# Performance work log

Hardware: AMD Instinct MI355X
Metric: run time of the kernel (lower is better)

The kernel has to match this reference:

```python
import jax, jax.numpy as jnp
import numpy as np

B, W, E, P, H, NH = 2, 512, 2, 8, 1024, 16
D = H // NH  # 64
T = W + E


def _split_heads(x):
    # [..., S, H] -> [..., NH, S, D]
    x = x.reshape(x.shape[:-1] + (NH, D))
    return jnp.swapaxes(x, -2, -3)


def setup_inputs() -> dict:
    key = jax.random.key(0)
    ks = jax.random.split(key, 16)
    s = 0.02
    inp = {
        "word_hidden_states": jax.random.normal(ks[0], (B, W, H), jnp.float32),
        "entity_hidden_states": jax.random.normal(ks[1], (B, P, E, H), jnp.float32),
        "attention_mask": jnp.zeros((B, 1, 1, T), jnp.float32),
        "q_w": jax.random.normal(ks[2], (H, H), jnp.float32) * s,
        "q_b": jnp.zeros((H,), jnp.float32),
        "k_w": jax.random.normal(ks[3], (H, H), jnp.float32) * s,
        "k_b": jnp.zeros((H,), jnp.float32),
        "v_w": jax.random.normal(ks[4], (H, H), jnp.float32) * s,
        "v_b": jnp.zeros((H,), jnp.float32),
        "w2e_w": jax.random.normal(ks[5], (H, H), jnp.float32) * s,
        "w2e_b": jnp.zeros((H,), jnp.float32),
        "e2w_w": jax.random.normal(ks[6], (H, H), jnp.float32) * s,
        "e2w_b": jnp.zeros((H,), jnp.float32),
        "e2e_w": jax.random.normal(ks[7], (H, H), jnp.float32) * s,
        "e2e_b": jnp.zeros((H,), jnp.float32),
    }
    return inp


def reference(word_hidden_states, entity_hidden_states, attention_mask,
              q_w, q_b, k_w, k_b, v_w, v_b,
              w2e_w, w2e_b, e2w_w, e2w_b, e2e_w, e2e_b):
    words = word_hidden_states          # [B, W, H]
    ents = entity_hidden_states         # [B, P, E, H]

    # Queries: words use `query` and `w2e_query`; entities use `e2w_query` and `e2e_query`.
    w2w_q = _split_heads(words @ q_w + q_b)      # [B, NH, W, D]
    w2e_q = _split_heads(words @ w2e_w + w2e_b)  # [B, NH, W, D]
    e2w_q = _split_heads(ents @ e2w_w + e2w_b)   # [B, P, NH, E, D]
    e2e_q = _split_heads(ents @ e2e_w + e2e_b)   # [B, P, NH, E, D]

    # Shared key/value projection on [expanded words ; entities]. Word K/V are
    # identical across pairs (expand), so compute once and broadcast.
    k_word = _split_heads(words @ k_w + k_b)     # [B, NH, W, D]
    k_ent = _split_heads(ents @ k_w + k_b)       # [B, P, NH, E, D]
    v_word = _split_heads(words @ v_w + v_b)     # [B, NH, W, D]
    v_ent = _split_heads(ents @ v_w + v_b)       # [B, P, NH, E, D]

    # Four block score matrices.
    s_w2w = jnp.einsum('bhqd,bhkd->bhqk', w2w_q, k_word)      # [B, NH, W, W]
    s_w2e = jnp.einsum('bhqd,bphkd->bphqk', w2e_q, k_ent)     # [B, P, NH, W, E]
    s_e2w = jnp.einsum('bphqd,bhkd->bphqk', e2w_q, k_word)    # [B, P, NH, E, W]
    s_e2e = jnp.einsum('bphqd,bphkd->bphqk', e2e_q, k_ent)    # [B, P, NH, E, E]

    word_scores = jnp.concatenate(
        [jnp.broadcast_to(s_w2w[:, None], (B, P, NH, W, W)), s_w2e], axis=-1)
    ent_scores = jnp.concatenate([s_e2w, s_e2e], axis=-1)
    scores = jnp.concatenate([word_scores, ent_scores], axis=-2)  # [B, P, NH, T, T]

    scale = jnp.asarray(1.0 / np.sqrt(D), scores.dtype)
    scores = scores * scale + attention_mask[:, None]  # mask broadcasts [B,1,1,1,T]
    probs = jax.nn.softmax(scores, axis=-1)  # dropout: eval mode (deterministic)

    v = jnp.concatenate(
        [jnp.broadcast_to(v_word[:, None], (B, P, NH, W, D)), v_ent], axis=-2)
    ctx = jnp.einsum('bphqk,bphkd->bphqd', probs, v)   # [B, P, NH, T, D]
    ctx = jnp.swapaxes(ctx, -2, -3).reshape(B, P, T, H)

    word_reps = ctx[:, :, :W, :]   # [B, P, W, H]
    ent_reps = ctx[:, :, W:, :]    # [B, P, E, H]
    return (word_reps, ent_reps)
```

## Files before the change

kernel.cpp:

```cpp
#include <hip/hip_runtime.h>
#include <hip/hip_bf16.h>

typedef __attribute__((ext_vector_type(8))) short s16x8;
typedef __attribute__((ext_vector_type(4))) float fx4;
typedef __attribute__((ext_vector_type(4))) unsigned int u32x4;
typedef unsigned short u16;
typedef unsigned int   u32;
typedef unsigned long long u64;

#define DI __device__ __forceinline__


DI float bf2f(u16 x){ u32 u = ((u32)x)<<16; float f; __builtin_memcpy(&f,&u,4); return f; }
DI u16 f2bf(float f){ u32 u; __builtin_memcpy(&u,&f,4); u = (u + 0x7fffu + ((u>>16)&1u))>>16; return (u16)u; }

DI fx4 mfma_16x16x32_bf16(s16x8 a, s16x8 b, fx4 c){
  return __builtin_amdgcn_mfma_f32_16x16x32_bf16(a,b,c,0,0,0);
}

__global__ __launch_bounds__(256) void k_prep(
    const float* __restrict__ s0, const float* __restrict__ s1, const float* __restrict__ s2,
    const float* __restrict__ s3, const float* __restrict__ s4, const float* __restrict__ s5,
    u16* __restrict__ dstbase,
    const float* __restrict__ words, u16* __restrict__ Xbf,
    const float* __restrict__ ents,  u16* __restrict__ Ebf)
{
  __shared__ __align__(16) u16 tile[64][72];
  int bx = blockIdx.x, tid = threadIdx.x;
  if(bx < 1536){
    int z = bx>>8, t = bx&255;
    const float* src = (z==0)?s0:(z==1)?s1:(z==2)?s2:(z==3)?s3:(z==4)?s4:s5;
    u16* dst = dstbase + (u64)z*1048576u;
    int kt = (t&15)*64, nt = (t>>4)*64;
    #pragma unroll
    for(int it=0; it<2; ++it){
      int c = it*256 + tid;
      int r = c>>3, col = (c&7)*8;
      const float* sp = src + (u64)(kt+r)*1024u + nt + col;
      fx4 a = *(const fx4*)sp;
      fx4 b = *(const fx4*)(sp+4);
      u16 o[8];
      o[0]=f2bf(a[0]); o[1]=f2bf(a[1]); o[2]=f2bf(a[2]); o[3]=f2bf(a[3]);
      o[4]=f2bf(b[0]); o[5]=f2bf(b[1]); o[6]=f2bf(b[2]); o[7]=f2bf(b[3]);
      __builtin_memcpy(&tile[r][col], o, 16);
    }
    __syncthreads();
    #pragma unroll
    for(int it=0; it<2; ++it){
      int c = it*256 + tid;
      int nr = c>>3, kc = (c&7)*8;
      u16 tmp[8];
      #pragma unroll
      for(int j=0;j<8;++j) tmp[j] = tile[kc+j][nr];
      u32x4 v; __builtin_memcpy(&v, tmp, 16);
      *(u32x4*)(dst + (u64)(nt+nr)*1024u + kt + kc) = v;
    }
  } else {
    const float* src; u16* dst; int i;
    if(bx < 2048){ src = words; dst = Xbf; i = ((bx-1536)*256 + tid)*8; }
    else         { src = ents;  dst = Ebf; i = ((bx-2048)*256 + tid)*8; }
    fx4 a = *(const fx4*)(src+i);
    fx4 b = *(const fx4*)(src+i+4);
    u16 o[8];
    o[0]=f2bf(a[0]); o[1]=f2bf(a[1]); o[2]=f2bf(a[2]); o[3]=f2bf(a[3]);
    o[4]=f2bf(b[0]); o[5]=f2bf(b[1]); o[6]=f2bf(b[2]); o[7]=f2bf(b[3]);
    u32x4 v; __builtin_memcpy(&v,o,16);
    *(u32x4*)(dst+i)=v;
  }
}

__global__ __launch_bounds__(256) void k_proj(
    const u16* __restrict__ Xbf, const u16* __restrict__ Ebf,
    const u16* __restrict__ wtq, const u16* __restrict__ wtw2e,
    const u16* __restrict__ wtk, const u16* __restrict__ wtv,
    const u16* __restrict__ wte2w, const u16* __restrict__ wte2e,
    const float* __restrict__ qb, const float* __restrict__ w2eb,
    const float* __restrict__ kb, const float* __restrict__ vb,
    const float* __restrict__ e2wb, const float* __restrict__ e2eb,
    u16* __restrict__ Qw, u16* __restrict__ Q2e, u16* __restrict__ Kwp, u16* __restrict__ VwTp,
    u16* __restrict__ Qe2w, u16* __restrict__ Qe2e, u16* __restrict__ Kep, u16* __restrict__ VeTp)
{
  __shared__ __align__(16) u16 XL[128*64];
  __shared__ __align__(16) u16 WL[128*64];
  int tid = threadIdx.x;
  int z = blockIdx.z;
  int wv = tid>>6, lane = tid&63, l15 = lane&15, g = lane>>4;

  if(blockIdx.y < 8){
    const u16* WT  = (z==0)?wtq:(z==1)?wtw2e:(z==2)?wtk:wtv;
    const float* bias = (z==0)?qb :(z==1)?w2eb :(z==2)?kb :vb;
    u16* out       = (z==0)?Qw :(z==1)?Q2e :(z==2)?Kwp :VwTp;
    int nt = blockIdx.x*64;
    int mt = blockIdx.y*128;
    int wr = (wv>>1)*64, wc = (wv&1)*32;
    fx4 acc[4][2] = {};
    u32x4 rx[4], rw[2];
    #pragma unroll
    for(int it=0; it<4; ++it){
      int c = it*256 + tid;
      int r = c>>3, cb = (c&7)*16, scb = cb ^ ((r&7)<<4);
      rx[it] = *(const u32x4*)((const char*)Xbf + ((u64)(mt+r)*1024u)*2u + scb);
    }
    #pragma unroll
    for(int it=0; it<2; ++it){
      int c = it*256 + tid;
      int r = c>>3, cb = (c&7)*16, scb = cb ^ ((r&7)<<4);
      rw[it] = *(const u32x4*)((const char*)WT + ((u64)(nt+r)*1024u)*2u + scb);
    }
    #pragma unroll
    for(int it=0; it<4; ++it) *(u32x4*)((char*)XL + (it*256+tid)*16) = rx[it];
    #pragma unroll
    for(int it=0; it<2; ++it) *(u32x4*)((char*)WL + (it*256+tid)*16) = rw[it];
    __syncthreads();
    for(int t=0; t<16; ++t){
      int kn = (t+1)*64;
      if(t < 15){
        #pragma unroll
        for(int it=0; it<4; ++it){
          int c = it*256 + tid;
          int r = c>>3, cb = (c&7)*16, scb = cb ^ ((r&7)<<4);
          rx[it] = *(const u32x4*)((const char*)Xbf + ((u64)(mt+r)*1024u + kn)*2u + scb);
        }
        #pragma unroll
        for(int it=0; it<2; ++it){
          int c = it*256 + tid;
          int r = c>>3, cb = (c&7)*16, scb = cb ^ ((r&7)<<4);
          rw[it] = *(const u32x4*)((const char*)WT + ((u64)(nt+r)*1024u + kn)*2u + scb);
        }
      }
      #pragma unroll
      for(int ks=0; ks<2; ++ks){
        s16x8 af[4], bfv[2];
        #pragma unroll
        for(int i=0;i<4;++i){
          int ra = wr + i*16 + l15;
          af[i]  = *(const s16x8*)((const char*)XL + ra*128 + ((ks*64 + g*16) ^ ((ra&7)<<4)));
        }
        #pragma unroll
        for(int j=0;j<2;++j){
          int rb = wc + j*16 + l15;
          bfv[j] = *(const s16x8*)((const char*)WL + rb*128 + ((ks*64 + g*16) ^ ((rb&7)<<4)));
        }
        #pragma unroll
        for(int i=0;i<4;++i)
          #pragma unroll
          for(int j=0;j<2;++j)
            acc[i][j] = mfma_16x16x32_bf16(af[i], bfv[j], acc[i][j]);
      }
      __syncthreads();
      if(t < 15){
        #pragma unroll
        for(int it=0; it<4; ++it) *(u32x4*)((char*)XL + (it*256+tid)*16) = rx[it];
        #pragma unroll
        for(int it=0; it<2; ++it) *(u32x4*)((char*)WL + (it*256+tid)*16) = rw[it];
        __syncthreads();
      }
    }
    bool vmode = (z==3);
    #pragma unroll
    for(int j=0;j<2;++j){
      int n = nt + wc + j*16 + l15;
      float bv = bias[n];
      int h = n>>6, d = n&63;
      #pragma unroll
      for(int i=0;i<4;++i){
        #pragma unroll
        for(int q=0;q<4;++q){
          int m = mt + wr + i*16 + g*4 + q;
          int bb = m>>9, wrow = m&511;
          float v = acc[i][j][q] + bv;
          u64 o = vmode ? (((u64)(bb*16+h)*64u + d)*512u + wrow)
                        : (((u64)(bb*16+h)*512u + wrow)*64u + d);
          out[o] = f2bf(v);
        }
      }
    }
  } else {
    if(blockIdx.x >= 8) return;
    const u16* WT  = (z==0)?wte2w:(z==1)?wte2e:(z==2)?wtk:wtv;
    const float* bias = (z==0)?e2wb :(z==1)?e2eb :(z==2)?kb :vb;
    u16* out       = (z==0)?Qe2w :(z==1)?Qe2e :(z==2)?Kep :VeTp;
    int nt = blockIdx.x*128;
    int wc = wv*32;
    fx4 acc[2][2] = {};
    for(int kk=0; kk<1024; kk+=64){
      {
        int r = tid>>3, cb = (tid&7)*16, scb = cb ^ ((r&7)<<4);
        *(u32x4*)((char*)XL + r*128 + cb) =
          *(const u32x4*)((const char*)Ebf + ((u64)r*1024u + kk)*2u + scb);
      }
      #pragma unroll
      for(int it=0; it<4; ++it){
        int c = it*256 + tid;
        int r = c>>3, cb = (c&7)*16, scb = cb ^ ((r&7)<<4);
        *(u32x4*)((char*)WL + r*128 + cb) =
          *(const u32x4*)((const char*)WT + ((u64)(nt+r)*1024u + kk)*2u + scb);
      }
      __syncthreads();
      #pragma unroll
      for(int ks=0; ks<2; ++ks){
        s16x8 af[2], bfv[2];
        #pragma unroll
        for(int i=0;i<2;++i){
          int ra = i*16 + l15;
          af[i]  = *(const s16x8*)((const char*)XL + ra*128 + ((ks*64 + g*16) ^ ((ra&7)<<4)));
          int rb = wc + i*16 + l15;
          bfv[i] = *(const s16x8*)((const char*)WL + rb*128 + ((ks*64 + g*16) ^ ((rb&7)<<4)));
        }
        #pragma unroll
        for(int i=0;i<2;++i)
          #pragma unroll
          for(int j=0;j<2;++j)
            acc[i][j] = mfma_16x16x32_bf16(af[i], bfv[j], acc[i][j]);
      }
      __syncthreads();
    }
    bool vmode = (z==3);
    #pragma unroll
    for(int j=0;j<2;++j){
      int n = nt + wc + j*16 + l15;
      float bv = bias[n];
      int h = n>>6, d = n&63;
      #pragma unroll
      for(int i=0;i<2;++i){
        #pragma unroll
        for(int q=0;q<4;++q){
          int m = i*16 + g*4 + q;
          int bb = m>>4, p = (m>>1)&7, e = m&1;
          float v = acc[i][j][q] + bv;
          u64 base = ((u64)(bb*8+p)*16u + h);
          u64 o = vmode ? ((base*64u + d)*2u + e)
                        : ((base*2u + e)*64u + d);
          out[o] = f2bf(v);
        }
      }
    }
  }
}

__global__ __launch_bounds__(256) void k_attn(
    const u16* __restrict__ Qw,  const u16* __restrict__ Q2e,
    const u16* __restrict__ Kw,  const u16* __restrict__ VwT,
    const u16* __restrict__ Ke,  const u16* __restrict__ VeT,
    const u16* __restrict__ Qe2w, const u16* __restrict__ Qe2e,
    const float* __restrict__ msk, float* __restrict__ outw, float* __restrict__ oute)
{
  const float scale = 0.125f;
  __shared__ __align__(16) u16 KL[64*64];
  __shared__ __align__(16) u16 VtL[64*64];
  __shared__ __align__(16) u16 PT[4][64][18];
  __shared__ __align__(16) float mask_lds[576];
  __shared__ __align__(16) float obuf[4][16][68];
  __shared__ float s_lds[2][516];
  __shared__ float red[2][8];
  int tid = threadIdx.x;
  int h = blockIdx.y, b = blockIdx.z;
  int wv = tid>>6, lane = tid&63, l15 = lane&15, g = lane>>4;

  if(blockIdx.x < 8){
    int qc = blockIdx.x;
    int q0 = qc*64 + wv*16;

    for(int i=tid;i<576;i+=256) mask_lds[i] = (i<514) ? msk[b*514+i] : 0.f;

    const u16* Qrow = Qw + ((u64)(b*16+h)*512u + q0 + l15)*64u;
    s16x8 qf0 = *(const s16x8*)(Qrow + g*8);
    s16x8 qf1 = *(const s16x8*)(Qrow + 32 + g*8);

    const char* Kpan = (const char*)(Kw  + (u64)(b*16+h)*512u*64u);
    const char* Vpan = (const char*)(VwT + (u64)(b*16+h)*64u*512u);

    float m_run = -3.0e38f, l_run = 0.f;
    fx4 oacc[4] = {};
    int swz = (l15&7)<<4;

    u32x4 rk[2], rv[2];
    #pragma unroll
    for(int it=0; it<2; ++it){
      int cc = it*256 + tid;
      int r = cc>>3, cb = (cc&7)*16, scb = cb ^ ((r&7)<<4);
      rk[it] = *(const u32x4*)(Kpan + (u64)r*128u + scb);
      rv[it] = *(const u32x4*)(Vpan + (u64)r*1024u + scb);
    }
    #pragma unroll
    for(int it=0; it<2; ++it){
      int cc = it*256 + tid;
      int r = cc>>3, cb = (cc&7)*16;
      *(u32x4*)((char*)KL  + r*128 + cb) = rk[it];
      *(u32x4*)((char*)VtL + r*128 + cb) = rv[it];
    }
    __syncthreads();

    for(int c=0;c<8;++c){
      if(c < 7){
        #pragma unroll
        for(int it=0; it<2; ++it){
          int cc = it*256 + tid;
          int r = cc>>3, cb = (cc&7)*16, scb = cb ^ ((r&7)<<4);
          rk[it] = *(const u32x4*)(Kpan + (u64)((c+1)*64+r)*128u + scb);
          rv[it] = *(const u32x4*)(Vpan + (u64)r*1024u + (u64)(c+1)*128u + scb);
        }
      }
      float sv[4][4];
      #pragma unroll
      for(int s=0;s<4;++s){
        int rk_ = (s*16 + l15)*128;
        s16x8 ka0 = *(const s16x8*)((const char*)KL + rk_ + ((g*16) ^ swz));
        s16x8 ka1 = *(const s16x8*)((const char*)KL + rk_ + ((64 + g*16) ^ swz));
        fx4 st = {0.f,0.f,0.f,0.f};
        st = mfma_16x16x32_bf16(ka0, qf0, st);
        st = mfma_16x16x32_bf16(ka1, qf1, st);
        fx4 mk = *(const fx4*)&mask_lds[c*64 + s*16 + g*4];
        #pragma unroll
        for(int q=0;q<4;++q) sv[s][q] = st[q]*scale + mk[q];
      }
      float cm = -3.0e38f;
      #pragma unroll
      for(int s=0;s<4;++s)
        #pragma unroll
        for(int q=0;q<4;++q) cm = fmaxf(cm, sv[s][q]);
      cm = fmaxf(cm, __shfl_xor(cm, 16, 64));
      cm = fmaxf(cm, __shfl_xor(cm, 32, 64));
      float m_new = fmaxf(m_run, cm);
      float alpha = __expf(m_run - m_new);
      float rs = 0.f;
      #pragma unroll
      for(int s=0;s<4;++s){
        #pragma unroll
        for(int q=0;q<4;++q){
          float e = __expf(sv[s][q] - m_new);
          rs += e;
          PT[wv][s*16 + g*4 + q][l15] = f2bf(e);
        }
      }
      rs += __shfl_xor(rs, 16, 64);
      rs += __shfl_xor(rs, 32, 64);
      l_run = l_run*alpha + rs;
      m_run = m_new;
      #pragma unroll
      for(int t=0;t<4;++t) oacc[t] *= alpha;
      asm volatile("s_waitcnt lgkmcnt(0)" ::: "memory");
      #pragma unroll
      for(int kh=0;kh<2;++kh){
        u16 ptmp[8];
        #pragma unroll
        for(int j=0;j<8;++j) ptmp[j] = PT[wv][kh*32 + g*8 + j][l15];
        s16x8 pbig; __builtin_memcpy(&pbig, ptmp, 16);
        #pragma unroll
        for(int t=0;t<4;++t){
          int rv_ = (t*16 + l15)*128;
          s16x8 va = *(const s16x8*)((const char*)VtL + rv_ + ((kh*64 + g*16) ^ swz));
          oacc[t] = mfma_16x16x32_bf16(va, pbig, oacc[t]);
        }
      }
      __syncthreads();
      if(c < 7){
        #pragma unroll
        for(int it=0; it<2; ++it){
          int cc = it*256 + tid;
          int r = cc>>3, cb = (cc&7)*16;
          *(u32x4*)((char*)KL  + r*128 + cb) = rk[it];
          *(u32x4*)((char*)VtL + r*128 + cb) = rv[it];
        }
        __syncthreads();
      }
    }

    #pragma unroll
    for(int t=0;t<4;++t)
      #pragma unroll
      for(int q=0;q<4;++q)
        obuf[wv][l15][t*16 + g*4 + q] = oacc[t][q];
    asm volatile("s_waitcnt lgkmcnt(0)" ::: "memory");

    int r = lane>>2, cbo = (lane&3)*16;
    fx4 N0 = *(const fx4*)&obuf[wv][r][cbo];
    fx4 N1 = *(const fx4*)&obuf[wv][r][cbo+4];
    fx4 N2 = *(const fx4*)&obuf[wv][r][cbo+8];
    fx4 N3 = *(const fx4*)&obuf[wv][r][cbo+12];
    float m_r = __shfl(m_run, r, 64);
    float l_r = __shfl(l_run, r, 64);
    float mke0 = mask_lds[512], mke1 = mask_lds[513];

    const u16* q2p = Q2e + ((u64)(b*16+h)*512u + q0 + r)*64u + cbo;
    float q2v[16];
    {
      s16x8 qa = *(const s16x8*)q2p;
      s16x8 qb2 = *(const s16x8*)(q2p+8);
      #pragma unroll
      for(int j=0;j<8;++j){ q2v[j]=bf2f((u16)qa[j]); q2v[8+j]=bf2f((u16)qb2[j]); }
    }

    for(int p=0;p<8;++p){
      const u16* KeP = Ke + ((u64)(b*8+p)*16u + h)*128u;
      float d0=0.f, d1=0.f;
      {
        const u16* k0p = KeP + cbo;
        const u16* k1p = KeP + 64 + cbo;
        s16x8 a0 = *(const s16x8*)k0p, a1 = *(const s16x8*)(k0p+8);
        s16x8 b0 = *(const s16x8*)k1p, b1 = *(const s16x8*)(k1p+8);
        #pragma unroll
        for(int j=0;j<8;++j){
          d0 += q2v[j]*bf2f((u16)a0[j]) + q2v[8+j]*bf2f((u16)a1[j]);
          d1 += q2v[j]*bf2f((u16)b0[j]) + q2v[8+j]*bf2f((u16)b1[j]);
        }
      }
      d0 += __shfl_xor(d0, 1, 64); d0 += __shfl_xor(d0, 2, 64);
      d1 += __shfl_xor(d1, 1, 64); d1 += __shfl_xor(d1, 2, 64);
      float s0 = d0*scale + mke0, s1 = d1*scale + mke1;
      float mp = fmaxf(m_r, fmaxf(s0, s1));
      float al = __expf(m_r - mp);
      float p0 = __expf(s0-mp), p1 = __expf(s1-mp);
      float linv = 1.0f/(l_r*al + p0 + p1);
      const u16* vep = VeT + ((u64)(b*8+p)*16u + h)*128u + cbo*2;
      u16 ve[32];
      {
        u32x4 w0 = *(const u32x4*)vep;
        u32x4 w1 = *(const u32x4*)(vep+8);
        u32x4 w2 = *(const u32x4*)(vep+16);
        u32x4 w3 = *(const u32x4*)(vep+24);
        __builtin_memcpy(ve,    &w0, 16);
        __builtin_memcpy(ve+8,  &w1, 16);
        __builtin_memcpy(ve+16, &w2, 16);
        __builtin_memcpy(ve+24, &w3, 16);
      }
      float o[16];
      #pragma unroll
      for(int j=0;j<4;++j){
        o[j]    = (N0[j]*al + p0*bf2f(ve[2*j])      + p1*bf2f(ve[2*j+1]))*linv;
        o[4+j]  = (N1[j]*al + p0*bf2f(ve[8+2*j])    + p1*bf2f(ve[8+2*j+1]))*linv;
        o[8+j]  = (N2[j]*al + p0*bf2f(ve[16+2*j])   + p1*bf2f(ve[16+2*j+1]))*linv;
        o[12+j] = (N3[j]*al + p0*bf2f(ve[24+2*j])   + p1*bf2f(ve[24+2*j+1]))*linv;
      }
      float* og = outw + ((u64)(b*8+p)*512u + q0 + r)*1024u + h*64 + cbo;
      *(fx4*)og      = *(const fx4*)&o[0];
      *(fx4*)(og+4)  = *(const fx4*)&o[4];
      *(fx4*)(og+8)  = *(const fx4*)&o[8];
      *(fx4*)(og+12) = *(const fx4*)&o[12];
    }
  } else {
    int p = blockIdx.x - 8;
    u64 ebase = (u64)(b*8+p)*16u + h;
    float* qw_lds = (float*)KL;
    float* qe_lds = (float*)VtL;
    if(tid < 128){
      int r = tid>>6, d = tid&63;
      qw_lds[r*64+d] = bf2f(Qe2w[(ebase*2 + r)*64 + d]);
      qe_lds[r*64+d] = bf2f(Qe2e[(ebase*2 + r)*64 + d]);
    }
    __syncthreads();
    const u16* Kpan = Kw + (u64)(b*16+h)*512u*64u;
    for(int k=tid;k<512;k+=256){
      const u16* kr = Kpan + (u64)k*64u;
      float d0=0.f, d1=0.f;
      #pragma unroll
      for(int j=0;j<64;j+=8){
        s16x8 kv = *(const s16x8*)(kr+j);
        #pragma unroll
        for(int x=0;x<8;++x){
          float kf = bf2f((u16)kv[x]);
          d0 += qw_lds[j+x]*kf;
          d1 += qw_lds[64+j+x]*kf;
        }
      }
      float mk = msk[b*514 + k];
      s_lds[0][k] = d0*0.125f + mk;
      s_lds[1][k] = d1*0.125f + mk;
    }
    if(tid < 4){
      int r = tid>>1, e = tid&1;
      const u16* kr = Ke + (ebase*2 + e)*64;
      float dd = 0.f;
      for(int j=0;j<64;++j) dd += qe_lds[r*64+j]*bf2f(kr[j]);
      s_lds[r][512+e] = dd*0.125f + msk[b*514 + 512 + e];
    }
    __syncthreads();
    float mx0=-3e38f, mx1=-3e38f;
    for(int k=tid;k<514;k+=256){ mx0=fmaxf(mx0,s_lds[0][k]); mx1=fmaxf(mx1,s_lds[1][k]); }
    #pragma unroll
    for(int off=32; off; off>>=1){
      mx0 = fmaxf(mx0, __shfl_xor(mx0, off, 64));
      mx1 = fmaxf(mx1, __shfl_xor(mx1, off, 64));
    }
    if(lane==0){ red[0][wv]=mx0; red[1][wv]=mx1; }
    __syncthreads();
    float m0 = fmaxf(fmaxf(red[0][0],red[0][1]),fmaxf(red[0][2],red[0][3]));
    float m1 = fmaxf(fmaxf(red[1][0],red[1][1]),fmaxf(red[1][2],red[1][3]));
    float sm0=0.f, sm1=0.f;
    for(int k=tid;k<514;k+=256){
      float e0 = __expf(s_lds[0][k]-m0); s_lds[0][k]=e0; sm0+=e0;
      float e1 = __expf(s_lds[1][k]-m1); s_lds[1][k]=e1; sm1+=e1;
    }
    #pragma unroll
    for(int off=32; off; off>>=1){
      sm0 += __shfl_xor(sm0, off, 64);
      sm1 += __shfl_xor(sm1, off, 64);
    }
    if(lane==0){ red[0][4+wv]=sm0; red[1][4+wv]=sm1; }
    __syncthreads();
    float l0 = red[0][4]+red[0][5]+red[0][6]+red[0][7];
    float l1 = red[1][4]+red[1][5]+red[1][6]+red[1][7];
    if(tid < 128){
      int r = tid>>6, d = tid&63;
      const u16* vr = VwT + ((u64)(b*16+h)*64u + d)*512u;
      float acc = 0.f;
      for(int k=0;k<512;k+=8){
        s16x8 vv = *(const s16x8*)(vr+k);
        #pragma unroll
        for(int x=0;x<8;++x) acc += s_lds[r][k+x]*bf2f((u16)vv[x]);
      }
      const u16* ve = VeT + (ebase*64 + d)*2;
      acc += s_lds[r][512]*bf2f(ve[0]) + s_lds[r][513]*bf2f(ve[1]);
      float val = acc / ((r==0)?l0:l1);
      oute[(((u64)(b*8+p)*2u + r)*1024u + h*64 + d)] = val;
    }
  }
}

extern "C" void kernel_launch(void* const* d_in, const int* in_sizes, int n_in,
                              void* d_out, int out_size, void* d_ws, size_t ws_size,
                              hipStream_t stream)
{
  const float* words = (const float*)d_in[0];
  const float* ents  = (const float*)d_in[1];
  const float* amask = (const float*)d_in[2];
  const float* q_w   = (const float*)d_in[3];
  const float* q_b   = (const float*)d_in[4];
  const float* k_w   = (const float*)d_in[5];
  const float* k_b   = (const float*)d_in[6];
  const float* v_w   = (const float*)d_in[7];
  const float* v_b   = (const float*)d_in[8];
  const float* w2e_w = (const float*)d_in[9];
  const float* w2e_b = (const float*)d_in[10];
  const float* e2w_w = (const float*)d_in[11];
  const float* e2w_b = (const float*)d_in[12];
  const float* e2e_w = (const float*)d_in[13];
  const float* e2e_b = (const float*)d_in[14];

  const size_t MW = 1048576;
  u16* ws16 = (u16*)d_ws;
  if(ws_size < (11*MW + 5*32768)*sizeof(u16)) return;
  u16* WTq   = ws16 + 0*MW;
  u16* WTk   = ws16 + 1*MW;
  u16* WTv   = ws16 + 2*MW;
  u16* WTw2e = ws16 + 3*MW;
  u16* WTe2w = ws16 + 4*MW;
  u16* WTe2e = ws16 + 5*MW;
  u16* Qw    = ws16 + 6*MW;
  u16* Q2e   = ws16 + 7*MW;
  u16* Kwp   = ws16 + 8*MW;
  u16* VwTp  = ws16 + 9*MW;
  u16* Xbf   = ws16 + 10*MW;
  u16* Qe2w  = ws16 + 11*MW;
  u16* Qe2e  = Qe2w + 32768;
  u16* Kep   = Qe2e + 32768;
  u16* VeTp  = Kep + 32768;
  u16* Ebf   = VeTp + 32768;

  dim3 tb(256);
  k_prep<<<dim3(2064), tb, 0, stream>>>(q_w, k_w, v_w, w2e_w, e2w_w, e2e_w, ws16,
                                        words, Xbf, ents, Ebf);
  k_proj<<<dim3(16,9,4), tb, 0, stream>>>(Xbf, Ebf,
      WTq, WTw2e, WTk, WTv, WTe2w, WTe2e,
      q_b, w2e_b, k_b, v_b, e2w_b, e2e_b,
      Qw, Q2e, Kwp, VwTp, Qe2w, Qe2e, Kep, VeTp);
  k_attn<<<dim3(16,16,2), tb, 0, stream>>>(Qw, Q2e, Kwp, VwTp, Kep, VeTp,
      Qe2w, Qe2e, amask, (float*)d_out, (float*)d_out + 8388608u);
}
```

Baseline: 65.27 us.

## Double-buffer LDS tiles with direct global-to-LDS loads in projection and attention

Replaces the register-staged prefetch (global load into registers, then LDS store after a barrier) with double-buffered LDS tiles filled by global_load_lds, in both the word projection GEMM and the word attention K/V loop. The goal is to remove the VGPR staging, the extra LDS write pass and one barrier per iteration, letting the next tile's loads overlap with the current MFMAs. It doubles LDS use for these buffers, which may lower occupancy. Correctness depends on the async LDS writes being complete at the single per-iteration __syncthreads, since no explicit vmcnt wait is added.

```diff
diff --git a/kernel.cpp b/kernel.cpp
--- a/kernel.cpp
+++ b/kernel.cpp
@@ -16,6 +16,12 @@
 
 DI fx4 mfma_16x16x32_bf16(s16x8 a, s16x8 b, fx4 c){
   return __builtin_amdgcn_mfma_f32_16x16x32_bf16(a,b,c,0,0,0);
+}
+
+DI void gload16(const void* g, void* l){
+  __builtin_amdgcn_global_load_lds(
+      (const __attribute__((address_space(1))) unsigned int*)g,
+      (__attribute__((address_space(3))) unsigned int*)l, 16, 0, 0);
 }
 
 __global__ __launch_bounds__(256) void k_prep(
@@ -80,8 +86,8 @@
     u16* __restrict__ Qw, u16* __restrict__ Q2e, u16* __restrict__ Kwp, u16* __restrict__ VwTp,
     u16* __restrict__ Qe2w, u16* __restrict__ Qe2e, u16* __restrict__ Kep, u16* __restrict__ VeTp)
 {
-  __shared__ __align__(16) u16 XL[128*64];
-  __shared__ __align__(16) u16 WL[128*64];
+  __shared__ __align__(16) u16 XL2[2][128*64];
+  __shared__ __align__(16) u16 WL2[2][64*64];
   int tid = threadIdx.x;
   int z = blockIdx.z;
   int wv = tid>>6, lane = tid&63, l15 = lane&15, g = lane>>4;
@@ -94,52 +100,42 @@
     int mt = blockIdx.y*128;
     int wr = (wv>>1)*64, wc = (wv&1)*32;
     fx4 acc[4][2] = {};
-    u32x4 rx[4], rw[2];
-    #pragma unroll
-    for(int it=0; it<4; ++it){
-      int c = it*256 + tid;
-      int r = c>>3, cb = (c&7)*16, scb = cb ^ ((r&7)<<4);
-      rx[it] = *(const u32x4*)((const char*)Xbf + ((u64)(mt+r)*1024u)*2u + scb);
-    }
-    #pragma unroll
-    for(int it=0; it<2; ++it){
-      int c = it*256 + tid;
-      int r = c>>3, cb = (c&7)*16, scb = cb ^ ((r&7)<<4);
-      rw[it] = *(const u32x4*)((const char*)WT + ((u64)(nt+r)*1024u)*2u + scb);
-    }
-    #pragma unroll
-    for(int it=0; it<4; ++it) *(u32x4*)((char*)XL + (it*256+tid)*16) = rx[it];
-    #pragma unroll
-    for(int it=0; it<2; ++it) *(u32x4*)((char*)WL + (it*256+tid)*16) = rw[it];
-    __syncthreads();
+
+    auto STAGE = [&](int t, int buf){
+      int kk = t*64;
+      #pragma unroll
+      for(int it=0;it<4;++it){
+        int c = it*256+tid; int r=c>>3, cb=(c&7)*16, scb=cb^((r&7)<<4);
+        gload16((const char*)Xbf + ((u64)(mt+r)*1024u + kk)*2u + scb,
+                (char*)XL2[buf] + c*16);
+      }
+      #pragma unroll
+      for(int it=0;it<2;++it){
+        int c = it*256+tid; int r=c>>3, cb=(c&7)*16, scb=cb^((r&7)<<4);
+        gload16((const char*)WT + ((u64)(nt+r)*1024u + kk)*2u + scb,
+                (char*)WL2[buf] + c*16);
+      }
+    };
+
+    STAGE(0, 0);
+    __syncthreads();
+    int cur = 0;
     for(int t=0; t<16; ++t){
-      int kn = (t+1)*64;
-      if(t < 15){
-        #pragma unroll
-        for(int it=0; it<4; ++it){
-          int c = it*256 + tid;
-          int r = c>>3, cb = (c&7)*16, scb = cb ^ ((r&7)<<4);
-          rx[it] = *(const u32x4*)((const char*)Xbf + ((u64)(mt+r)*1024u + kn)*2u + scb);
-        }
-        #pragma unroll
-        for(int it=0; it<2; ++it){
-          int c = it*256 + tid;
-          int r = c>>3, cb = (c&7)*16, scb = cb ^ ((r&7)<<4);
-          rw[it] = *(const u32x4*)((const char*)WT + ((u64)(nt+r)*1024u + kn)*2u + scb);
-        }
-      }
+      if(t < 15) STAGE(t+1, cur^1);
+      const char* XB = (const char*)XL2[cur];
+      const char* WB = (const char*)WL2[cur];
       #pragma unroll
       for(int ks=0; ks<2; ++ks){
         s16x8 af[4], bfv[2];
         #pragma unroll
         for(int i=0;i<4;++i){
           int ra = wr + i*16 + l15;
-          af[i]  = *(const s16x8*)((const char*)XL + ra*128 + ((ks*64 + g*16) ^ ((ra&7)<<4)));
+          af[i]  = *(const s16x8*)(XB + ra*128 + ((ks*64 + g*16) ^ ((ra&7)<<4)));
         }
         #pragma unroll
         for(int j=0;j<2;++j){
           int rb = wc + j*16 + l15;
-          bfv[j] = *(const s16x8*)((const char*)WL + rb*128 + ((ks*64 + g*16) ^ ((rb&7)<<4)));
+          bfv[j] = *(const s16x8*)(WB + rb*128 + ((ks*64 + g*16) ^ ((rb&7)<<4)));
         }
         #pragma unroll
         for(int i=0;i<4;++i)
@@ -148,13 +144,7 @@
             acc[i][j] = mfma_16x16x32_bf16(af[i], bfv[j], acc[i][j]);
       }
       __syncthreads();
-      if(t < 15){
-        #pragma unroll
-        for(int it=0; it<4; ++it) *(u32x4*)((char*)XL + (it*256+tid)*16) = rx[it];
-        #pragma unroll
-        for(int it=0; it<2; ++it) *(u32x4*)((char*)WL + (it*256+tid)*16) = rw[it];
-        __syncthreads();
-      }
+      cur ^= 1;
     }
     bool vmode = (z==3);
     #pragma unroll
@@ -180,20 +170,22 @@
     const u16* WT  = (z==0)?wte2w:(z==1)?wte2e:(z==2)?wtk:wtv;
     const float* bias = (z==0)?e2wb :(z==1)?e2eb :(z==2)?kb :vb;
     u16* out       = (z==0)?Qe2w :(z==1)?Qe2e :(z==2)?Kep :VeTp;
+    char* XLe = (char*)XL2;
+    char* WLe = (char*)WL2;
     int nt = blockIdx.x*128;
     int wc = wv*32;
     fx4 acc[2][2] = {};
     for(int kk=0; kk<1024; kk+=64){
       {
         int r = tid>>3, cb = (tid&7)*16, scb = cb ^ ((r&7)<<4);
-        *(u32x4*)((char*)XL + r*128 + cb) =
+        *(u32x4*)(XLe + r*128 + cb) =
           *(const u32x4*)((const char*)Ebf + ((u64)r*1024u + kk)*2u + scb);
       }
       #pragma unroll
       for(int it=0; it<4; ++it){
         int c = it*256 + tid;
         int r = c>>3, cb = (c&7)*16, scb = cb ^ ((r&7)<<4);
-        *(u32x4*)((char*)WL + r*128 + cb) =
+        *(u32x4*)(WLe + r*128 + cb) =
           *(const u32x4*)((const char*)WT + ((u64)(nt+r)*1024u + kk)*2u + scb);
       }
       __syncthreads();
@@ -203,9 +195,9 @@
         #pragma unroll
         for(int i=0;i<2;++i){
           int ra = i*16 + l15;
-          af[i]  = *(const s16x8*)((const char*)XL + ra*128 + ((ks*64 + g*16) ^ ((ra&7)<<4)));
+          af[i]  = *(const s16x8*)(XLe + ra*128 + ((ks*64 + g*16) ^ ((ra&7)<<4)));
           int rb = wc + i*16 + l15;
-          bfv[i] = *(const s16x8*)((const char*)WL + rb*128 + ((ks*64 + g*16) ^ ((rb&7)<<4)));
+          bfv[i] = *(const s16x8*)(WLe + rb*128 + ((ks*64 + g*16) ^ ((rb&7)<<4)));
         }
         #pragma unroll
         for(int i=0;i<2;++i)
@@ -246,8 +238,8 @@
     const float* __restrict__ msk, float* __restrict__ outw, float* __restrict__ oute)
 {
   const float scale = 0.125f;
-  __shared__ __align__(16) u16 KL[64*64];
-  __shared__ __align__(16) u16 VtL[64*64];
+  __shared__ __align__(16) u16 KL2[2][64*64];
+  __shared__ __align__(16) u16 VtL2[2][64*64];
   __shared__ __align__(16) u16 PT[4][64][18];
   __shared__ __align__(16) float mask_lds[576];
   __shared__ __align__(16) float obuf[4][16][68];
@@ -261,52 +253,41 @@
     int qc = blockIdx.x;
     int q0 = qc*64 + wv*16;
 
+    const char* Kpan = (const char*)(Kw  + (u64)(b*16+h)*512u*64u);
+    const char* Vpan = (const char*)(VwT + (u64)(b*16+h)*64u*512u);
+
+    auto STAGEC = [&](int c, int buf){
+      #pragma unroll
+      for(int it=0;it<2;++it){
+        int cc = it*256+tid; int r=cc>>3, cb=(cc&7)*16, scb=cb^((r&7)<<4);
+        gload16(Kpan + (u64)(c*64+r)*128u + scb, (char*)KL2[buf] + cc*16);
+        gload16(Vpan + (u64)r*1024u + (u64)c*128u + scb, (char*)VtL2[buf] + cc*16);
+      }
+    };
+
+    STAGEC(0, 0);
     for(int i=tid;i<576;i+=256) mask_lds[i] = (i<514) ? msk[b*514+i] : 0.f;
 
     const u16* Qrow = Qw + ((u64)(b*16+h)*512u + q0 + l15)*64u;
     s16x8 qf0 = *(const s16x8*)(Qrow + g*8);
     s16x8 qf1 = *(const s16x8*)(Qrow + 32 + g*8);
 
-    const char* Kpan = (const char*)(Kw  + (u64)(b*16+h)*512u*64u);
-    const char* Vpan = (const char*)(VwT + (u64)(b*16+h)*64u*512u);
-
     float m_run = -3.0e38f, l_run = 0.f;
     fx4 oacc[4] = {};
     int swz = (l15&7)<<4;
-
-    u32x4 rk[2], rv[2];
-    #pragma unroll
-    for(int it=0; it<2; ++it){
-      int cc = it*256 + tid;
-      int r = cc>>3, cb = (cc&7)*16, scb = cb ^ ((r&7)<<4);
-      rk[it] = *(const u32x4*)(Kpan + (u64)r*128u + scb);
-      rv[it] = *(const u32x4*)(Vpan + (u64)r*1024u + scb);
-    }
-    #pragma unroll
-    for(int it=0; it<2; ++it){
-      int cc = it*256 + tid;
-      int r = cc>>3, cb = (cc&7)*16;
-      *(u32x4*)((char*)KL  + r*128 + cb) = rk[it];
-      *(u32x4*)((char*)VtL + r*128 + cb) = rv[it];
-    }
-    __syncthreads();
-
+    __syncthreads();
+
+    int cur = 0;
     for(int c=0;c<8;++c){
-      if(c < 7){
-        #pragma unroll
-        for(int it=0; it<2; ++it){
-          int cc = it*256 + tid;
-          int r = cc>>3, cb = (cc&7)*16, scb = cb ^ ((r&7)<<4);
-          rk[it] = *(const u32x4*)(Kpan + (u64)((c+1)*64+r)*128u + scb);
-          rv[it] = *(const u32x4*)(Vpan + (u64)r*1024u + (u64)(c+1)*128u + scb);
-        }
-      }
+      if(c < 7) STAGEC(c+1, cur^1);
+      const char* KB = (const char*)KL2[cur];
+      const char* VB = (const char*)VtL2[cur];
       float sv[4][4];
       #pragma unroll
       for(int s=0;s<4;++s){
         int rk_ = (s*16 + l15)*128;
-        s16x8 ka0 = *(const s16x8*)((const char*)KL + rk_ + ((g*16) ^ swz));
-        s16x8 ka1 = *(const s16x8*)((const char*)KL + rk_ + ((64 + g*16) ^ swz));
+        s16x8 ka0 = *(const s16x8*)(KB + rk_ + ((g*16) ^ swz));
+        s16x8 ka1 = *(const s16x8*)(KB + rk_ + ((64 + g*16) ^ swz));
         fx4 st = {0.f,0.f,0.f,0.f};
         st = mfma_16x16x32_bf16(ka0, qf0, st);
         st = mfma_16x16x32_bf16(ka1, qf1, st);
@@ -349,21 +330,12 @@
         #pragma unroll
         for(int t=0;t<4;++t){
           int rv_ = (t*16 + l15)*128;
-          s16x8 va = *(const s16x8*)((const char*)VtL + rv_ + ((kh*64 + g*16) ^ swz));
+          s16x8 va = *(const s16x8*)(VB + rv_ + ((kh*64 + g*16) ^ swz));
           oacc[t] = mfma_16x16x32_bf16(va, pbig, oacc[t]);
         }
       }
       __syncthreads();
-      if(c < 7){
-        #pragma unroll
-        for(int it=0; it<2; ++it){
-          int cc = it*256 + tid;
-          int r = cc>>3, cb = (cc&7)*16;
-          *(u32x4*)((char*)KL  + r*128 + cb) = rk[it];
-          *(u32x4*)((char*)VtL + r*128 + cb) = rv[it];
-        }
-        __syncthreads();
-      }
+      cur ^= 1;
     }
 
     #pragma unroll
@@ -441,8 +413,8 @@
   } else {
     int p = blockIdx.x - 8;
     u64 ebase = (u64)(b*8+p)*16u + h;
-    float* qw_lds = (float*)KL;
-    float* qe_lds = (float*)VtL;
+    float* qw_lds = (float*)KL2;
+    float* qe_lds = (float*)VtL2;
     if(tid < 128){
       int r = tid>>6, d = tid&63;
       qw_lds[r*64+d] = bf2f(Qe2w[(ebase*2 + r)*64 + d]);
```

Measured after the change: 66.52 us. No clear change (+1.9%).
